# Kernel tuning notes

Measured on AMD Instinct MI355X. Metric: run time of the kernel, lower is better.

Reference implementation:

```python
import jax, jax.numpy as jnp
import numpy as np

EMBED = 1024
HEADS = 16
HEAD_DIM = EMBED // HEADS


def setup_inputs() -> dict:
    key = jax.random.key(0)
    k1, k2, k3, k4, k5 = jax.random.split(key, 5)
    N, S = 2, 2048
    values = jax.random.normal(k1, (N, S, EMBED), dtype=jnp.float32)
    keys = jax.random.normal(k2, (N, S, EMBED), dtype=jnp.float32)
    query = jax.random.normal(k3, (N, S, EMBED), dtype=jnp.float32)
    mask = jnp.ones((N, 1, S, S), dtype=jnp.int32)
    # fc_out: Linear(heads*head_dim, embed_size) with bias; torch stores W as [out, in]
    W_out = jax.random.normal(k4, (EMBED, EMBED), dtype=jnp.float32) / np.sqrt(EMBED)
    b_out = jax.random.normal(k5, (EMBED,), dtype=jnp.float32) * 0.01
    return {"values": values, "keys": keys, "query": query, "mask": mask,
            "W_out": W_out, "b_out": b_out}


def reference(values, keys, query, mask, W_out, b_out):
    N, S, E = query.shape
    H, D = HEADS, HEAD_DIM
    # NOTE: source module never applies its q/k/v Linear layers (bug preserved).
    v = values.reshape(N, S, H, D)
    k = keys.reshape(N, S, H, D)
    q = query.reshape(N, S, H, D)
    energy = jnp.einsum('nqhd,nkhd->nhqk', q, k)  # [N,H,S,S]
    energy = jnp.where(mask == 0, jnp.float32(-1e20), energy)
    # non-standard scale: sqrt(embed_size), faithful to source
    attn = jax.nn.softmax(energy / jnp.sqrt(jnp.float32(E)), axis=3)
    out = jnp.einsum('nhql,nlhd->nqhd', attn, v).reshape(N, S, H * D)
    return out @ W_out.T + b_out
```

## Files before the change

kernel.cpp:

```cpp
#include <hip/hip_runtime.h>
#include <stdint.h>

#define S_LEN 2048
#define EMB 1024
#define NHEADS 16
#define HD 64
#define LOG2E 1.4426950408889634f

typedef __bf16 bf16x8 __attribute__((ext_vector_type(8)));
typedef float f32x4 __attribute__((ext_vector_type(4)));
typedef unsigned short u16;

#define MFMA16(a, b, c) __builtin_amdgcn_mfma_f32_16x16x32_bf16(a, b, c, 0, 0, 0)
#define GLOAD_LDS16(gp, lp)                                        \
  __builtin_amdgcn_global_load_lds(                                \
      (const __attribute__((address_space(1))) unsigned int*)(gp), \
      (__attribute__((address_space(3))) unsigned int*)(lp), 16, 0, 0)

__device__ __forceinline__ u16 bf16r(float x) {
  union { float f; unsigned int u; } c; c.f = x;
  unsigned int u = c.u + 0x7fffu + ((c.u >> 16) & 1u);
  return (u16)(u >> 16);
}

__device__ __forceinline__ unsigned int cvt_pk_bf16(float lo, float hi) {
  unsigned int r;
  asm("v_cvt_pk_bf16_f32 %0, %1, %2" : "=v"(r) : "v"(lo), "v"(hi));
  return r;
}

__device__ __forceinline__ float fexp2(float x) {
  float r;
  asm("v_exp_f32 %0, %1" : "=v"(r) : "v"(x));
  return r;
}

__device__ __forceinline__ int kperm(int k) {
  int kb = (k >> 4) & 3, g = (k >> 2) & 3, r = k & 3;
  return (kb >> 1) * 32 + g * 8 + (kb & 1) * 4 + r;
}

__global__ __launch_bounds__(256) void prep_kernel(
    const float* __restrict__ values, const float* __restrict__ keys,
    const float* __restrict__ W, const int* __restrict__ mask,
    u16* __restrict__ vt, u16* __restrict__ kb, u16* __restrict__ wb,
    unsigned char* __restrict__ fl2) {
  __shared__ u16 tile[64][65];
  __shared__ int s_ok[4];
  int b = blockIdx.x;
  int t = threadIdx.x;
  if (b < 1024) {
    int st = b & 31, h = (b >> 5) & 15, n = b >> 9;
    int s0 = st * 64;
    int d = t & 63, r4 = t >> 6;
#pragma unroll
    for (int i = 0; i < 16; ++i) {
      int s = r4 + i * 4;
      float x = values[(size_t)(n * S_LEN + s0 + s) * EMB + h * HD + d];
      tile[s][d] = bf16r(x);
    }
    __syncthreads();
    int sp = s0 + kperm(d);
#pragma unroll
    for (int i = 0; i < 16; ++i) {
      int dd = r4 + i * 4;
      vt[(size_t)((n * NHEADS + h) * HD + dd) * S_LEN + sp] = tile[d][dd];
    }
  } else if (b < 2048) {
    int idx = (b - 1024) * 256 + t;
    const float4* in4 = (const float4*)keys;
    ushort4* out4 = (ushort4*)kb;
#pragma unroll
    for (int j = 0; j < 4; ++j) {
      float4 v = in4[idx + j * 262144];
      ushort4 o;
      o.x = bf16r(v.x); o.y = bf16r(v.y); o.z = bf16r(v.z); o.w = bf16r(v.w);
      out4[idx + j * 262144] = o;
    }
  } else if (b < 2304) {
    int idx = (b - 2048) * 256 + t;
    const float4* in4 = (const float4*)W;
    ushort4* out4 = (ushort4*)wb;
#pragma unroll
    for (int j = 0; j < 4; ++j) {
      float4 v = in4[idx + j * 65536];
      ushort4 o;
      o.x = bf16r(v.x); o.y = bf16r(v.y); o.z = bf16r(v.z); o.w = bf16r(v.w);
      out4[idx + j * 65536] = o;
    }
  } else {
    int idx = b - 2304;
    int kt = idx & 31, qt = (idx >> 5) & 15, n = idx >> 9;
    int qr = t >> 1, c8 = t & 1;
    const int4* mp = (const int4*)(mask + (size_t)n * S_LEN * S_LEN +
                                   (size_t)(qt * 128 + qr) * S_LEN + kt * 64) + c8 * 8;
    int ok = 1;
#pragma unroll
    for (int i = 0; i < 8; ++i) {
      int4 m = mp[i];
      ok &= (m.x != 0) & (m.y != 0) & (m.z != 0) & (m.w != 0);
    }
    ok = __all(ok);
    if ((t & 63) == 0) s_ok[t >> 6] = ok;
    __syncthreads();
    if (t == 0) fl2[idx] = (unsigned char)(s_ok[0] & s_ok[1] & s_ok[2] & s_ok[3]);
  }
}

__global__ __launch_bounds__(256, 4) void attn_kernel(
    const float* __restrict__ query, const u16* __restrict__ kbuf,
    const u16* __restrict__ vt, const int* __restrict__ mask,
    const unsigned char* __restrict__ fl2, u16* __restrict__ ob) {
  __shared__ __align__(16) unsigned char kl[2][8192];
  __shared__ __align__(16) unsigned char vl[2][8192];

  int b = blockIdx.x;
  b = (b & 7) * 128 + (b >> 3);
  int qt = b & 31, h = (b >> 5) & 15, n = b >> 9;
  int t = threadIdx.x, w = t >> 6, l = t & 63, l16 = l & 15, g = l >> 4;
  int q0w = qt * 64 + w * 16;

  bf16x8 aq[2];
#pragma unroll
  for (int hh = 0; hh < 2; ++hh) {
    const float* qp = query + (size_t)(n * S_LEN + q0w + l16) * EMB + h * HD + hh * 32 + g * 8;
    float4 f0 = *(const float4*)qp;
    float4 f1 = *(const float4*)(qp + 4);
    union { bf16x8 v; unsigned int u32[4]; } qq;
    qq.u32[0] = cvt_pk_bf16(f0.x * 0.03125f, f0.y * 0.03125f);
    qq.u32[1] = cvt_pk_bf16(f0.z * 0.03125f, f0.w * 0.03125f);
    qq.u32[2] = cvt_pk_bf16(f1.x * 0.03125f, f1.y * 0.03125f);
    qq.u32[3] = cvt_pk_bf16(f1.z * 0.03125f, f1.w * 0.03125f);
    aq[hh] = qq.v;
  }

  f32x4 zero4 = {0.f, 0.f, 0.f, 0.f};
  f32x4 acc[4];
  float lrun = 0.f, mrun = 0.f, mL = 0.f;
#pragma unroll
  for (int db = 0; db < 4; ++db) acc[db] = zero4;

  int row_s = t >> 3, cc = t & 7;
  int sc = cc ^ (row_s & 7);
  const u16* gk0 = kbuf + (size_t)(n * S_LEN + row_s) * EMB + h * HD + sc * 8;
  const u16* gv0 = vt + (size_t)((n * NHEADS + h) * HD + row_s) * S_LEN + sc * 8;

  auto stage = [&](int kt, int nb) {
    const u16* gk = gk0 + (size_t)kt * 64 * EMB;
    const u16* gv = gv0 + kt * 64;
    GLOAD_LDS16(gk, kl[nb] + (w * 64) * 16);
    GLOAD_LDS16(gk + 32 * EMB, kl[nb] + (256 + w * 64) * 16);
    GLOAD_LDS16(gv, vl[nb] + (w * 64) * 16);
    GLOAD_LDS16(gv + 32 * S_LEN, vl[nb] + (256 + w * 64) * 16);
  };

  stage(0, 0);
  __syncthreads();

  for (int kt = 0; kt < S_LEN / 64; ++kt) {
    int cur = kt & 1;
    if (kt + 1 < S_LEN / 64) stage(kt + 1, cur ^ 1);
    const unsigned char* kc = kl[cur];
    const unsigned char* vc = vl[cur];

    f32x4 sf[4];
    __builtin_amdgcn_s_setprio(1);
#pragma unroll
    for (int kb = 0; kb < 4; ++kb) {
      int row = kb * 16 + l16;
      const unsigned char* kr = kc + row * 128;
      int sw = (row & 7) << 4;
      bf16x8 bk0 = *(const bf16x8*)(kr + ((g * 16) ^ sw));
      bf16x8 bk1 = *(const bf16x8*)(kr + ((64 + g * 16) ^ sw));
      f32x4 z = zero4;
      z = MFMA16(bk0, aq[0], z);
      z = MFMA16(bk1, aq[1], z);
      sf[kb] = z;
    }
    __builtin_amdgcn_s_setprio(0);

    unsigned char fflag = fl2[((n * 16 + (qt >> 1)) * 32) + kt];
    if (!fflag) {
      const int* mrow = mask + (size_t)n * S_LEN * S_LEN +
                        (size_t)(q0w + l16) * S_LEN + kt * 64 + g * 4;
#pragma unroll
      for (int kb = 0; kb < 4; ++kb) {
        int4 mm = *(const int4*)(mrow + kb * 16);
        if (mm.x == 0) sf[kb][0] = -30.f;
        if (mm.y == 0) sf[kb][1] = -30.f;
        if (mm.z == 0) sf[kb][2] = -30.f;
        if (mm.w == 0) sf[kb][3] = -30.f;
      }
    }

    float lmax = sf[0][0];
#pragma unroll
    for (int kb = 0; kb < 4; ++kb)
#pragma unroll
      for (int r = 0; r < 4; ++r) lmax = fmaxf(lmax, sf[kb][r]);
    if (!__all(lmax <= mrun + 8.f)) {
      float rmax = fmaxf(lmax, __shfl_xor(lmax, 16));
      rmax = fmaxf(rmax, __shfl_xor(rmax, 32));
      float Mn = fmaxf(mrun, rmax);
      float corr = fexp2((mrun - Mn) * LOG2E);
      mrun = Mn;
      mL = Mn * LOG2E;
      lrun *= corr;
#pragma unroll
      for (int r = 0; r < 4; ++r) {
        float ca = __shfl(corr, (l & 48) + (g << 2) + r);
#pragma unroll
        for (int db = 0; db < 4; ++db) acc[db][r] *= ca;
      }
    }
    float p[4][4];
#pragma unroll
    for (int kb = 0; kb < 4; ++kb)
#pragma unroll
      for (int r = 0; r < 4; ++r)
        p[kb][r] = fexp2(fmaf(sf[kb][r], LOG2E, -mL));
    float s01 = (p[0][0] + p[0][1]) + (p[0][2] + p[0][3]);
    float s23 = (p[1][0] + p[1][1]) + (p[1][2] + p[1][3]);
    float s45 = (p[2][0] + p[2][1]) + (p[2][2] + p[2][3]);
    float s67 = (p[3][0] + p[3][1]) + (p[3][2] + p[3][3]);
    lrun += (s01 + s23) + (s45 + s67);

    bf16x8 pa[2];
#pragma unroll
    for (int hh = 0; hh < 2; ++hh) {
      union { bf16x8 v; unsigned int u32[4]; } pp;
      pp.u32[0] = cvt_pk_bf16(p[2 * hh][0], p[2 * hh][1]);
      pp.u32[1] = cvt_pk_bf16(p[2 * hh][2], p[2 * hh][3]);
      pp.u32[2] = cvt_pk_bf16(p[2 * hh + 1][0], p[2 * hh + 1][1]);
      pp.u32[3] = cvt_pk_bf16(p[2 * hh + 1][2], p[2 * hh + 1][3]);
      pa[hh] = pp.v;
    }

    __builtin_amdgcn_s_setprio(1);
#pragma unroll
    for (int hh = 0; hh < 2; ++hh)
#pragma unroll
      for (int db = 0; db < 4; ++db) {
        int d = db * 16 + l16;
        bf16x8 bv = *(const bf16x8*)(vc + d * 128 + ((hh * 64 + g * 16) ^ ((d & 7) << 4)));
        acc[db] = MFMA16(pa[hh], bv, acc[db]);
      }
    __builtin_amdgcn_s_setprio(0);

    __syncthreads();
  }

  float s = lrun;
  s += __shfl_xor(s, 16);
  s += __shfl_xor(s, 32);
  float rinv[4];
#pragma unroll
  for (int r = 0; r < 4; ++r) {
    float sr = __shfl(s, (l & 48) + (g << 2) + r);
    rinv[r] = 1.f / sr;
  }
#pragma unroll
  for (int db = 0; db < 4; ++db)
#pragma unroll
    for (int r = 0; r < 4; ++r) {
      int qg = q0w + (g << 2) + r;
      ob[(size_t)(n * S_LEN + qg) * EMB + h * HD + db * 16 + l16] =
          bf16r(acc[db][r] * rinv[r]);
    }
}

__global__ __launch_bounds__(256) void proj_kernel(
    const u16* __restrict__ A, const u16* __restrict__ Bt,
    const float* __restrict__ bias, float* __restrict__ C) {
  __shared__ __align__(16) unsigned char al[2][16384];
  __shared__ __align__(16) unsigned char bl[2][16384];
  int bm = blockIdx.x, bn = blockIdx.y;
  int t = threadIdx.x, w = t >> 6, l = t & 63;
  int l16 = l & 15, g = l >> 4;
  int wm = w >> 1, wn = w & 1;
  f32x4 zero4 = {0.f, 0.f, 0.f, 0.f};
  f32x4 acc[4][4];
#pragma unroll
  for (int m = 0; m < 4; ++m)
#pragma unroll
    for (int nn = 0; nn < 4; ++nn) acc[m][nn] = zero4;
  int row_s = t >> 3, cc = t & 7;
  int sc = cc ^ (row_s & 7);
  const u16* ga0 = A + (size_t)(bm * 128 + row_s) * EMB + sc * 8;
  const u16* gb0 = Bt + (size_t)(bn * 128 + row_s) * EMB + sc * 8;

  auto stage = [&](int ks, int nb) {
#pragma unroll
    for (int i = 0; i < 4; ++i) {
      GLOAD_LDS16(ga0 + (size_t)i * 32 * EMB + ks * 64, al[nb] + (i * 256 + w * 64) * 16);
      GLOAD_LDS16(gb0 + (size_t)i * 32 * EMB + ks * 64, bl[nb] + (i * 256 + w * 64) * 16);
    }
  };

  stage(0, 0);
  __syncthreads();

  for (int ks = 0; ks < 16; ++ks) {
    int cur = ks & 1;
    if (ks + 1 < 16) stage(ks + 1, cur ^ 1);
    __builtin_amdgcn_s_setprio(1);
#pragma unroll
    for (int hh = 0; hh < 2; ++hh) {
      bf16x8 af[4], bfr[4];
#pragma unroll
      for (int m = 0; m < 4; ++m) {
        int row = wm * 64 + m * 16 + l16;
        af[m] = *(const bf16x8*)(al[cur] + row * 128 + ((hh * 64 + g * 16) ^ ((row & 7) << 4)));
      }
#pragma unroll
      for (int nn = 0; nn < 4; ++nn) {
        int row = wn * 64 + nn * 16 + l16;
        bfr[nn] = *(const bf16x8*)(bl[cur] + row * 128 + ((hh * 64 + g * 16) ^ ((row & 7) << 4)));
      }
#pragma unroll
      for (int m = 0; m < 4; ++m)
#pragma unroll
        for (int nn = 0; nn < 4; ++nn) acc[m][nn] = MFMA16(af[m], bfr[nn], acc[m][nn]);
    }
    __builtin_amdgcn_s_setprio(0);
    __syncthreads();
  }
#pragma unroll
  for (int nn = 0; nn < 4; ++nn) {
    int j = bn * 128 + wn * 64 + nn * 16 + l16;
    float bj = bias[j];
#pragma unroll
    for (int m = 0; m < 4; ++m) {
      int i0 = bm * 128 + wm * 64 + m * 16 + g * 4;
#pragma unroll
      for (int r = 0; r < 4; ++r) C[(size_t)(i0 + r) * EMB + j] = acc[m][nn][r] + bj;
    }
  }
}

extern "C" void kernel_launch(void* const* d_in, const int* in_sizes, int n_in,
                              void* d_out, int out_size, void* d_ws, size_t ws_size,
                              hipStream_t stream) {
  const float* values = (const float*)d_in[0];
  const float* keys = (const float*)d_in[1];
  const float* query = (const float*)d_in[2];
  const int* mask = (const int*)d_in[3];
  const float* W = (const float*)d_in[4];
  const float* bias = (const float*)d_in[5];
  float* out = (float*)d_out;

  u16* kb = (u16*)d_ws;
  u16* vt = kb + 4194304;
  u16* ob = vt + 4194304;
  u16* wb = ob + 4194304;
  unsigned char* fl2 = (unsigned char*)(wb + 1048576);

  prep_kernel<<<3328, 256, 0, stream>>>(values, keys, W, mask, vt, kb, wb, fl2);
  attn_kernel<<<1024, 256, 0, stream>>>(query, kb, vt, mask, fl2, ob);
  proj_kernel<<<dim3(32, 8), 256, 0, stream>>>(ob, wb, bias, out);
}
```

Baseline: 96.85 us.

## Switch attention to 32x32 MFMA with two-wave blocks and halve projection N-tile

The attention kernel moves from 16x16x32 to 32x32x16 bf16 MFMA, with each of two waves owning 32 query rows. It folds log2e into the query scale so the softmax exponent becomes a plain subtraction, and re-permutes the V transpose layout to match the new fragment order. The projection kernel uses 128x64 tiles over a 32x16 grid to raise block count. Bigger MFMA tiles cut LDS fragment reads per FLOP, but 128-thread blocks under launch_bounds(128,2) raise register pressure and may lower occupancy.

```diff
diff --git a/kernel.cpp b/kernel.cpp
--- a/kernel.cpp
+++ b/kernel.cpp
@@ -9,9 +9,11 @@
 
 typedef __bf16 bf16x8 __attribute__((ext_vector_type(8)));
 typedef float f32x4 __attribute__((ext_vector_type(4)));
+typedef float f32x16 __attribute__((ext_vector_type(16)));
 typedef unsigned short u16;
 
 #define MFMA16(a, b, c) __builtin_amdgcn_mfma_f32_16x16x32_bf16(a, b, c, 0, 0, 0)
+#define MFMA32(a, b, c) __builtin_amdgcn_mfma_f32_32x32x16_bf16(a, b, c, 0, 0, 0)
 #define GLOAD_LDS16(gp, lp)                                        \
   __builtin_amdgcn_global_load_lds(                                \
       (const __attribute__((address_space(1))) unsigned int*)(gp), \
@@ -35,9 +37,8 @@
   return r;
 }
 
-__device__ __forceinline__ int kperm(int k) {
-  int kb = (k >> 4) & 3, g = (k >> 2) & 3, r = k & 3;
-  return (kb >> 1) * 32 + g * 8 + (kb & 1) * 4 + r;
+__device__ __forceinline__ int sigma64(int s) {
+  return (s & ~12) | ((s & 4) << 1) | ((s & 8) >> 1);
 }
 
 __global__ __launch_bounds__(256) void prep_kernel(
@@ -60,7 +61,7 @@
       tile[s][d] = bf16r(x);
     }
     __syncthreads();
-    int sp = s0 + kperm(d);
+    int sp = s0 + sigma64(d);
 #pragma unroll
     for (int i = 0; i < 16; ++i) {
       int dd = r4 + i * 4;
@@ -107,7 +108,7 @@
   }
 }
 
-__global__ __launch_bounds__(256, 4) void attn_kernel(
+__global__ __launch_bounds__(128, 2) void attn_kernel(
     const float* __restrict__ query, const u16* __restrict__ kbuf,
     const u16* __restrict__ vt, const int* __restrict__ mask,
     const unsigned char* __restrict__ fl2, u16* __restrict__ ob) {
@@ -117,28 +118,29 @@
   int b = blockIdx.x;
   b = (b & 7) * 128 + (b >> 3);
   int qt = b & 31, h = (b >> 5) & 15, n = b >> 9;
-  int t = threadIdx.x, w = t >> 6, l = t & 63, l16 = l & 15, g = l >> 4;
-  int q0w = qt * 64 + w * 16;
-
-  bf16x8 aq[2];
-#pragma unroll
-  for (int hh = 0; hh < 2; ++hh) {
-    const float* qp = query + (size_t)(n * S_LEN + q0w + l16) * EMB + h * HD + hh * 32 + g * 8;
-    float4 f0 = *(const float4*)qp;
-    float4 f1 = *(const float4*)(qp + 4);
+  int t = threadIdx.x, w = t >> 6, l = t & 63;
+  int l31 = l & 31, lh = l >> 5;
+  int q0 = qt * 64 + w * 32;
+
+  const float QS = 0.03125f * LOG2E;
+  bf16x8 qf[4];
+  const float* qp = query + (size_t)(n * S_LEN + q0 + l31) * EMB + h * HD + lh * 8;
+#pragma unroll
+  for (int dj = 0; dj < 4; ++dj) {
+    float4 f0 = *(const float4*)(qp + dj * 16);
+    float4 f1 = *(const float4*)(qp + dj * 16 + 4);
     union { bf16x8 v; unsigned int u32[4]; } qq;
-    qq.u32[0] = cvt_pk_bf16(f0.x * 0.03125f, f0.y * 0.03125f);
-    qq.u32[1] = cvt_pk_bf16(f0.z * 0.03125f, f0.w * 0.03125f);
-    qq.u32[2] = cvt_pk_bf16(f1.x * 0.03125f, f1.y * 0.03125f);
-    qq.u32[3] = cvt_pk_bf16(f1.z * 0.03125f, f1.w * 0.03125f);
-    aq[hh] = qq.v;
-  }
-
-  f32x4 zero4 = {0.f, 0.f, 0.f, 0.f};
-  f32x4 acc[4];
-  float lrun = 0.f, mrun = 0.f, mL = 0.f;
-#pragma unroll
-  for (int db = 0; db < 4; ++db) acc[db] = zero4;
+    qq.u32[0] = cvt_pk_bf16(f0.x * QS, f0.y * QS);
+    qq.u32[1] = cvt_pk_bf16(f0.z * QS, f0.w * QS);
+    qq.u32[2] = cvt_pk_bf16(f1.x * QS, f1.y * QS);
+    qq.u32[3] = cvt_pk_bf16(f1.z * QS, f1.w * QS);
+    qf[dj] = qq.v;
+  }
+
+  f32x16 zero16 = {0.f, 0.f, 0.f, 0.f, 0.f, 0.f, 0.f, 0.f,
+                   0.f, 0.f, 0.f, 0.f, 0.f, 0.f, 0.f, 0.f};
+  f32x16 acc0 = zero16, acc1 = zero16;
+  float lrun = 0.f, mrun = 0.f;
 
   int row_s = t >> 3, cc = t & 7;
   int sc = cc ^ (row_s & 7);
@@ -148,10 +150,11 @@
   auto stage = [&](int kt, int nb) {
     const u16* gk = gk0 + (size_t)kt * 64 * EMB;
     const u16* gv = gv0 + kt * 64;
-    GLOAD_LDS16(gk, kl[nb] + (w * 64) * 16);
-    GLOAD_LDS16(gk + 32 * EMB, kl[nb] + (256 + w * 64) * 16);
-    GLOAD_LDS16(gv, vl[nb] + (w * 64) * 16);
-    GLOAD_LDS16(gv + 32 * S_LEN, vl[nb] + (256 + w * 64) * 16);
+#pragma unroll
+    for (int i = 0; i < 4; ++i) {
+      GLOAD_LDS16(gk + (size_t)i * 16 * EMB, kl[nb] + i * 2048 + w * 1024);
+      GLOAD_LDS16(gv + i * 16 * S_LEN, vl[nb] + i * 2048 + w * 1024);
+    }
   };
 
   stage(0, 0);
@@ -163,138 +166,158 @@
     const unsigned char* kc = kl[cur];
     const unsigned char* vc = vl[cur];
 
-    f32x4 sf[4];
+    f32x16 s0 = zero16, s1 = zero16;
     __builtin_amdgcn_s_setprio(1);
-#pragma unroll
-    for (int kb = 0; kb < 4; ++kb) {
-      int row = kb * 16 + l16;
+    {
+      int row = l31;
       const unsigned char* kr = kc + row * 128;
       int sw = (row & 7) << 4;
-      bf16x8 bk0 = *(const bf16x8*)(kr + ((g * 16) ^ sw));
-      bf16x8 bk1 = *(const bf16x8*)(kr + ((64 + g * 16) ^ sw));
-      f32x4 z = zero4;
-      z = MFMA16(bk0, aq[0], z);
-      z = MFMA16(bk1, aq[1], z);
-      sf[kb] = z;
+#pragma unroll
+      for (int dj = 0; dj < 4; ++dj) {
+        bf16x8 ka = *(const bf16x8*)(kr + ((dj * 32 + lh * 16) ^ sw));
+        s0 = MFMA32(ka, qf[dj], s0);
+      }
+      const unsigned char* kr1 = kc + (32 + row) * 128;
+#pragma unroll
+      for (int dj = 0; dj < 4; ++dj) {
+        bf16x8 ka = *(const bf16x8*)(kr1 + ((dj * 32 + lh * 16) ^ sw));
+        s1 = MFMA32(ka, qf[dj], s1);
+      }
     }
     __builtin_amdgcn_s_setprio(0);
 
-    unsigned char fflag = fl2[((n * 16 + (qt >> 1)) * 32) + kt];
-    if (!fflag) {
+    unsigned char ff = fl2[((n * 16 + (qt >> 1)) * 32) + kt];
+    if (!ff) {
       const int* mrow = mask + (size_t)n * S_LEN * S_LEN +
-                        (size_t)(q0w + l16) * S_LEN + kt * 64 + g * 4;
-#pragma unroll
-      for (int kb = 0; kb < 4; ++kb) {
-        int4 mm = *(const int4*)(mrow + kb * 16);
-        if (mm.x == 0) sf[kb][0] = -30.f;
-        if (mm.y == 0) sf[kb][1] = -30.f;
-        if (mm.z == 0) sf[kb][2] = -30.f;
-        if (mm.w == 0) sf[kb][3] = -30.f;
-      }
-    }
-
-    float lmax = sf[0][0];
-#pragma unroll
-    for (int kb = 0; kb < 4; ++kb)
-#pragma unroll
-      for (int r = 0; r < 4; ++r) lmax = fmaxf(lmax, sf[kb][r]);
+                        (size_t)(q0 + l31) * S_LEN + kt * 64 + lh * 4;
+#pragma unroll
+      for (int bq = 0; bq < 4; ++bq) {
+        int4 m0 = *(const int4*)(mrow + bq * 8);
+        int4 m1 = *(const int4*)(mrow + 32 + bq * 8);
+        if (m0.x == 0) s0[4 * bq + 0] = -100.f;
+        if (m0.y == 0) s0[4 * bq + 1] = -100.f;
+        if (m0.z == 0) s0[4 * bq + 2] = -100.f;
+        if (m0.w == 0) s0[4 * bq + 3] = -100.f;
+        if (m1.x == 0) s1[4 * bq + 0] = -100.f;
+        if (m1.y == 0) s1[4 * bq + 1] = -100.f;
+        if (m1.z == 0) s1[4 * bq + 2] = -100.f;
+        if (m1.w == 0) s1[4 * bq + 3] = -100.f;
+      }
+    }
+
+    float mx0 = fmaxf(s0[0], s0[1]), mx1 = fmaxf(s0[2], s0[3]);
+    float mx2 = fmaxf(s0[4], s0[5]), mx3 = fmaxf(s0[6], s0[7]);
+#pragma unroll
+    for (int i = 8; i < 16; i += 4) {
+      mx0 = fmaxf(mx0, fmaxf(s0[i], s0[i + 1]));
+      mx1 = fmaxf(mx1, fmaxf(s0[i + 2], s0[i + 3]));
+    }
+#pragma unroll
+    for (int i = 0; i < 16; i += 4) {
+      mx2 = fmaxf(mx2, fmaxf(s1[i], s1[i + 1]));
+      mx3 = fmaxf(mx3, fmaxf(s1[i + 2], s1[i + 3]));
+    }
+    float lmax = fmaxf(fmaxf(mx0, mx1), fmaxf(mx2, mx3));
     if (!__all(lmax <= mrun + 8.f)) {
-      float rmax = fmaxf(lmax, __shfl_xor(lmax, 16));
-      rmax = fmaxf(rmax, __shfl_xor(rmax, 32));
+      float rmax = fmaxf(lmax, __shfl_xor(lmax, 32));
       float Mn = fmaxf(mrun, rmax);
-      float corr = fexp2((mrun - Mn) * LOG2E);
+      float corr = fexp2(mrun - Mn);
       mrun = Mn;
-      mL = Mn * LOG2E;
       lrun *= corr;
 #pragma unroll
-      for (int r = 0; r < 4; ++r) {
-        float ca = __shfl(corr, (l & 48) + (g << 2) + r);
-#pragma unroll
-        for (int db = 0; db < 4; ++db) acc[db][r] *= ca;
-      }
-    }
-    float p[4][4];
-#pragma unroll
-    for (int kb = 0; kb < 4; ++kb)
-#pragma unroll
-      for (int r = 0; r < 4; ++r)
-        p[kb][r] = fexp2(fmaf(sf[kb][r], LOG2E, -mL));
-    float s01 = (p[0][0] + p[0][1]) + (p[0][2] + p[0][3]);
-    float s23 = (p[1][0] + p[1][1]) + (p[1][2] + p[1][3]);
-    float s45 = (p[2][0] + p[2][1]) + (p[2][2] + p[2][3]);
-    float s67 = (p[3][0] + p[3][1]) + (p[3][2] + p[3][3]);
-    lrun += (s01 + s23) + (s45 + s67);
-
-    bf16x8 pa[2];
-#pragma unroll
-    for (int hh = 0; hh < 2; ++hh) {
+      for (int r = 0; r < 16; ++r) {
+        float ca = __shfl(corr, (r & 3) + 8 * (r >> 2) + 4 * lh);
+        acc0[r] *= ca;
+        acc1[r] *= ca;
+      }
+    }
+
+    float p0[16], p1[16];
+#pragma unroll
+    for (int i = 0; i < 16; ++i) p0[i] = fexp2(s0[i] - mrun);
+#pragma unroll
+    for (int i = 0; i < 16; ++i) p1[i] = fexp2(s1[i] - mrun);
+    float q4[8];
+#pragma unroll
+    for (int i = 0; i < 4; ++i)
+      q4[i] = (p0[4 * i] + p0[4 * i + 1]) + (p0[4 * i + 2] + p0[4 * i + 3]);
+#pragma unroll
+    for (int i = 0; i < 4; ++i)
+      q4[4 + i] = (p1[4 * i] + p1[4 * i + 1]) + (p1[4 * i + 2] + p1[4 * i + 3]);
+    lrun += ((q4[0] + q4[1]) + (q4[2] + q4[3])) + ((q4[4] + q4[5]) + (q4[6] + q4[7]));
+
+    bf16x8 pa[4];
+#pragma unroll
+    for (int j = 0; j < 4; ++j) {
+      const float* ps = (j < 2) ? p0 : p1;
+      int o = (j & 1) * 8;
       union { bf16x8 v; unsigned int u32[4]; } pp;
-      pp.u32[0] = cvt_pk_bf16(p[2 * hh][0], p[2 * hh][1]);
-      pp.u32[1] = cvt_pk_bf16(p[2 * hh][2], p[2 * hh][3]);
-      pp.u32[2] = cvt_pk_bf16(p[2 * hh + 1][0], p[2 * hh + 1][1]);
-      pp.u32[3] = cvt_pk_bf16(p[2 * hh + 1][2], p[2 * hh + 1][3]);
-      pa[hh] = pp.v;
+      pp.u32[0] = cvt_pk_bf16(ps[o + 0], ps[o + 1]);
+      pp.u32[1] = cvt_pk_bf16(ps[o + 2], ps[o + 3]);
+      pp.u32[2] = cvt_pk_bf16(ps[o + 4], ps[o + 5]);
+      pp.u32[3] = cvt_pk_bf16(ps[o + 6], ps[o + 7]);
+      pa[j] = pp.v;
     }
 
     __builtin_amdgcn_s_setprio(1);
-#pragma unroll
-    for (int hh = 0; hh < 2; ++hh)
-#pragma unroll
-      for (int db = 0; db < 4; ++db) {
-        int d = db * 16 + l16;
-        bf16x8 bv = *(const bf16x8*)(vc + d * 128 + ((hh * 64 + g * 16) ^ ((d & 7) << 4)));
-        acc[db] = MFMA16(pa[hh], bv, acc[db]);
-      }
+    {
+      const unsigned char* vr = vc + l31 * 128;
+      int sw = (l31 & 7) << 4;
+#pragma unroll
+      for (int j = 0; j < 4; ++j) {
+        bf16x8 bv = *(const bf16x8*)(vr + ((j * 32 + lh * 16) ^ sw));
+        acc0 = MFMA32(pa[j], bv, acc0);
+      }
+      const unsigned char* vr1 = vc + (32 + l31) * 128;
+#pragma unroll
+      for (int j = 0; j < 4; ++j) {
+        bf16x8 bv = *(const bf16x8*)(vr1 + ((j * 32 + lh * 16) ^ sw));
+        acc1 = MFMA32(pa[j], bv, acc1);
+      }
+    }
     __builtin_amdgcn_s_setprio(0);
 
     __syncthreads();
   }
 
-  float s = lrun;
-  s += __shfl_xor(s, 16);
-  s += __shfl_xor(s, 32);
-  float rinv[4];
-#pragma unroll
-  for (int r = 0; r < 4; ++r) {
-    float sr = __shfl(s, (l & 48) + (g << 2) + r);
-    rinv[r] = 1.f / sr;
-  }
-#pragma unroll
-  for (int db = 0; db < 4; ++db)
-#pragma unroll
-    for (int r = 0; r < 4; ++r) {
-      int qg = q0w + (g << 2) + r;
-      ob[(size_t)(n * S_LEN + qg) * EMB + h * HD + db * 16 + l16] =
-          bf16r(acc[db][r] * rinv[r]);
-    }
+  float ltot = lrun + __shfl_xor(lrun, 32);
+  float own_rinv = 1.f / ltot;
+#pragma unroll
+  for (int r = 0; r < 16; ++r) {
+    int qr = (r & 3) + 8 * (r >> 2) + 4 * lh;
+    float rinv = __shfl(own_rinv, qr);
+    size_t base = (size_t)(n * S_LEN + q0 + qr) * EMB + h * HD;
+    ob[base + l31] = bf16r(acc0[r] * rinv);
+    ob[base + 32 + l31] = bf16r(acc1[r] * rinv);
+  }
 }
 
 __global__ __launch_bounds__(256) void proj_kernel(
     const u16* __restrict__ A, const u16* __restrict__ Bt,
     const float* __restrict__ bias, float* __restrict__ C) {
   __shared__ __align__(16) unsigned char al[2][16384];
-  __shared__ __align__(16) unsigned char bl[2][16384];
+  __shared__ __align__(16) unsigned char bl[2][8192];
   int bm = blockIdx.x, bn = blockIdx.y;
   int t = threadIdx.x, w = t >> 6, l = t & 63;
   int l16 = l & 15, g = l >> 4;
-  int wm = w >> 1, wn = w & 1;
   f32x4 zero4 = {0.f, 0.f, 0.f, 0.f};
-  f32x4 acc[4][4];
-#pragma unroll
-  for (int m = 0; m < 4; ++m)
-#pragma unroll
-    for (int nn = 0; nn < 4; ++nn) acc[m][nn] = zero4;
+  f32x4 acc[2][4];
+#pragma unroll
+  for (int mi = 0; mi < 2; ++mi)
+#pragma unroll
+    for (int nj = 0; nj < 4; ++nj) acc[mi][nj] = zero4;
   int row_s = t >> 3, cc = t & 7;
   int sc = cc ^ (row_s & 7);
   const u16* ga0 = A + (size_t)(bm * 128 + row_s) * EMB + sc * 8;
-  const u16* gb0 = Bt + (size_t)(bn * 128 + row_s) * EMB + sc * 8;
+  const u16* gb0 = Bt + (size_t)(bn * 64 + row_s) * EMB + sc * 8;
 
   auto stage = [&](int ks, int nb) {
 #pragma unroll
-    for (int i = 0; i < 4; ++i) {
+    for (int i = 0; i < 4; ++i)
       GLOAD_LDS16(ga0 + (size_t)i * 32 * EMB + ks * 64, al[nb] + (i * 256 + w * 64) * 16);
+#pragma unroll
+    for (int i = 0; i < 2; ++i)
       GLOAD_LDS16(gb0 + (size_t)i * 32 * EMB + ks * 64, bl[nb] + (i * 256 + w * 64) * 16);
-    }
   };
 
   stage(0, 0);
@@ -306,34 +329,34 @@
     __builtin_amdgcn_s_setprio(1);
 #pragma unroll
     for (int hh = 0; hh < 2; ++hh) {
-      bf16x8 af[4], bfr[4];
-#pragma unroll
-      for (int m = 0; m < 4; ++m) {
-        int row = wm * 64 + m * 16 + l16;
-        af[m] = *(const bf16x8*)(al[cur] + row * 128 + ((hh * 64 + g * 16) ^ ((row & 7) << 4)));
-      }
-#pragma unroll
-      for (int nn = 0; nn < 4; ++nn) {
-        int row = wn * 64 + nn * 16 + l16;
-        bfr[nn] = *(const bf16x8*)(bl[cur] + row * 128 + ((hh * 64 + g * 16) ^ ((row & 7) << 4)));
-      }
-#pragma unroll
-      for (int m = 0; m < 4; ++m)
-#pragma unroll
-        for (int nn = 0; nn < 4; ++nn) acc[m][nn] = MFMA16(af[m], bfr[nn], acc[m][nn]);
+      bf16x8 af[2], bfr[4];
+#pragma unroll
+      for (int mi = 0; mi < 2; ++mi) {
+        int row = w * 32 + mi * 16 + l16;
+        af[mi] = *(const bf16x8*)(al[cur] + row * 128 + ((hh * 64 + g * 16) ^ ((row & 7) << 4)));
+      }
+#pragma unroll
+      for (int nj = 0; nj < 4; ++nj) {
+        int row = nj * 16 + l16;
+        bfr[nj] = *(const bf16x8*)(bl[cur] + row * 128 + ((hh * 64 + g * 16) ^ ((row & 7) << 4)));
+      }
+#pragma unroll
+      for (int mi = 0; mi < 2; ++mi)
+#pragma unroll
+        for (int nj = 0; nj < 4; ++nj) acc[mi][nj] = MFMA16(af[mi], bfr[nj], acc[mi][nj]);
     }
     __builtin_amdgcn_s_setprio(0);
     __syncthreads();
   }
 #pragma unroll
-  for (int nn = 0; nn < 4; ++nn) {
-    int j = bn * 128 + wn * 64 + nn * 16 + l16;
+  for (int nj = 0; nj < 4; ++nj) {
+    int j = bn * 64 + nj * 16 + l16;
     float bj = bias[j];
 #pragma unroll
-    for (int m = 0; m < 4; ++m) {
-      int i0 = bm * 128 + wm * 64 + m * 16 + g * 4;
-#pragma unroll
-      for (int r = 0; r < 4; ++r) C[(size_t)(i0 + r) * EMB + j] = acc[m][nn][r] + bj;
+    for (int mi = 0; mi < 2; ++mi) {
+      int i0 = bm * 128 + w * 32 + mi * 16 + g * 4;
+#pragma unroll
+      for (int r = 0; r < 4; ++r) C[(size_t)(i0 + r) * EMB + j] = acc[mi][nj][r] + bj;
     }
   }
 }
@@ -356,6 +379,6 @@
   unsigned char* fl2 = (unsigned char*)(wb + 1048576);
 
   prep_kernel<<<3328, 256, 0, stream>>>(values, keys, W, mask, vt, kb, wb, fl2);
-  attn_kernel<<<1024, 256, 0, stream>>>(query, kb, vt, mask, fl2, ob);
-  proj_kernel<<<dim3(32, 8), 256, 0, stream>>>(ob, wb, bias, out);
-}
+  attn_kernel<<<1024, 128, 0, stream>>>(query, kb, vt, mask, fl2, ob);
+  proj_kernel<<<dim3(32, 16), 256, 0, stream>>>(ob, wb, bias, out);
+}
```

After: 105.2 us. 1.09x slower.
